# Kernel tuning notes

Measured on AMD Instinct MI355X. Metric: run time of the kernel, lower is better.

## Reference

```python
import jax, jax.numpy as jnp
import numpy as np
from jax.scipy.special import gammaln, logsumexp

N, P, K, R = 100000, 256, 64, 16

def setup_inputs() -> dict:
    key = jax.random.key(0)
    kx, km, kp = jax.random.split(key, 3)
    X = jax.random.normal(kx, (N, P), dtype=jnp.float32)
    X = X / jnp.linalg.norm(X, axis=1, keepdims=True)  # points on the sphere S^{p-1}
    M = jax.random.normal(km, (K, P, R), dtype=jnp.float32)
    pi = jax.random.normal(kp, (K,), dtype=jnp.float32)
    return {"X": X, "M": M, "pi": pi}

def reference(X, M, pi):
    p = X.shape[1]
    r = M.shape[-1]
    half_p = 0.5 * float(p)
    # log surface area constant of the ACG normalizer
    logSA = gammaln(half_p) - jnp.log(2.0) - half_p * jnp.log(jnp.pi)
    # D = I_r + M^T M per component: [K, r, r]
    D = jnp.eye(r, dtype=M.dtype) + jnp.einsum('kpr,kps->krs', M, M)
    _, log_det_D = jnp.linalg.slogdet(D)            # [K]
    Dinv = jnp.linalg.inv(D)                        # [K, r, r]
    XM = jnp.einsum('np,kpr->knr', X, M)            # [K, N, r]
    quad = jnp.einsum('knr,krs,kns->kn', XM, Dinv, XM)  # [K, N]
    pdf = 1.0 - quad                                # Woodbury: x^T Sigma^{-1} x for unit x
    log_acg_pdf = logSA - 0.5 * log_det_D[:, None] - half_p * jnp.log(pdf)
    density = log_acg_pdf + jax.nn.log_softmax(pi)[:, None]   # [K, N]
    loglik = jnp.sum(logsumexp(density, axis=0))
    return loglik
```

## Files before the change

kernel.cpp:

```cpp
#include <hip/hip_runtime.h>
#include <hip/hip_bf16.h>
#include <math.h>

#define NPTS 100000
#define NSTRIPE 1568
#define KCOMP 64

typedef float v4f __attribute__((ext_vector_type(4)));
typedef __bf16 v8bf __attribute__((ext_vector_type(8)));
typedef __bf16 v4bf __attribute__((ext_vector_type(4)));


__global__ __launch_bounds__(256) void prep_comp(const float* __restrict__ M,
                                                 const float* __restrict__ pi,
                                                 __bf16* __restrict__ Bt,
                                                 float* __restrict__ cvec,
                                                 float logSA) {
    __shared__ float Ml[256][16];
    __shared__ float S[16][17];
    __shared__ float sh_logpi;
    const int k = blockIdx.x, t = threadIdx.x;

    const float4* src = (const float4*)(M + (size_t)k * 4096 + (size_t)t * 16);
    float4 a0 = src[0], a1 = src[1], a2 = src[2], a3 = src[3];
    ((float4*)Ml[t])[0] = a0; ((float4*)Ml[t])[1] = a1;
    ((float4*)Ml[t])[2] = a2; ((float4*)Ml[t])[3] = a3;

    if (t < 64) {
        float v = pi[t];
        float mx = v;
        for (int off = 32; off; off >>= 1) mx = fmaxf(mx, __shfl_xor(mx, off));
        float e = __expf(v - mx);
        float s = e;
        for (int off = 32; off; off >>= 1) s += __shfl_xor(s, off);
        if (t == 0) sh_logpi = pi[k] - mx - logf(s);
    }
    __syncthreads();

    {
        int r = t >> 4, c = t & 15;
        float s = (r == c) ? 1.0f : 0.0f;
        for (int p = 0; p < 256; ++p) s += Ml[p][r] * Ml[p][c];
        S[r][c] = s;
    }
    __syncthreads();

    for (int j = 0; j < 16; ++j) {
        if (t == 0) S[j][j] = sqrtf(S[j][j]);
        __syncthreads();
        if (t > j && t < 16) S[t][j] = S[t][j] / S[j][j];
        __syncthreads();
        {
            int r = t >> 4, c = t & 15;
            if (r > j && c > j && c <= r) S[r][c] -= S[r][j] * S[c][j];
        }
        __syncthreads();
    }

    if (t == 0) {
        float ldet = 0.0f;
        for (int j = 0; j < 16; ++j) ldet += logf(S[j][j]);
        cvec[k] = logSA - ldet + sh_logpi;
    }

    float m[16] = {a0.x, a0.y, a0.z, a0.w, a1.x, a1.y, a1.z, a1.w,
                   a2.x, a2.y, a2.z, a2.w, a3.x, a3.y, a3.z, a3.w};
    float y[16];
#pragma unroll
    for (int r = 0; r < 16; ++r) {
        float v = m[r];
#pragma unroll
        for (int q = 0; q < r; ++q) v -= S[r][q] * y[q];
        y[r] = v / S[r][r];
    }
    const int cw = k >> 2, n = k & 3;
    const int ks = t >> 5, e = t & 7;
    const int lbase = ((t >> 3) & 3) * 16;
#pragma unroll
    for (int r = 0; r < 16; ++r) {
        const size_t off = (size_t)cw * 16384 + (size_t)ks * 2048 + (size_t)n * 512
                         + (size_t)(lbase + r) * 8 + e;
        Bt[off] = (__bf16)y[r];
    }
}

__global__ __launch_bounds__(256) void convert_X(const float* __restrict__ X,
                                                 __bf16* __restrict__ Xb) {
    __shared__ __bf16 T[64][264];
    const int st = blockIdx.x;
    const int n0 = st * 64;
    const int t = threadIdx.x;

#pragma unroll
    for (int j = 0; j < 16; ++j) {
        const int u = j * 256 + t;
        const int r = u >> 6, c4 = u & 63;
        const int n = n0 + r;
        float4 v = make_float4(0.f, 0.f, 0.f, 0.f);
        if (n < NPTS) v = ((const float4*)X)[(size_t)n * 64 + c4];
        v4bf o = {(__bf16)v.x, (__bf16)v.y, (__bf16)v.z, (__bf16)v.w};
        *(v4bf*)&T[r][c4 * 4] = o;
    }
    __syncthreads();

#pragma unroll
    for (int ks = 0; ks < 8; ++ks) {
        const int mh = t >> 6;
        const int l = t & 63;
        const int row = mh * 16 + (l & 15);
        const int col = ks * 32 + (l >> 4) * 8;
        v8bf val = *(const v8bf*)&T[row][col];
        const size_t off = (size_t)st * 16384 + (size_t)ks * 2048
                         + (size_t)mh * 512 + (size_t)l * 8;
        *(v8bf*)(Xb + off) = val;
    }
}

__global__ __launch_bounds__(256, 2) void gemm_density(const __bf16* __restrict__ Xb,
                                                       const __bf16* __restrict__ Bt,
                                                       const float* __restrict__ cvec,
                                                       float* __restrict__ out) {
    const int bid = blockIdx.x;
    const int xcd = bid & 7;
    const int w = threadIdx.x >> 6, lane = threadIdx.x & 63;
    const int widx = (bid >> 3) * 4 + w;
    if (widx >= 196) return;
    const int st = xcd * 196 + widx;
    const int laneoff = lane * 8;

    const __bf16* Ab = Xb + ((size_t)st << 14) + laneoff;
    v8bf af[8][4];
#pragma unroll
    for (int ks = 0; ks < 8; ++ks)
#pragma unroll
        for (int m = 0; m < 4; ++m) {
            af[ks][m] = *(const v8bf*)(Ab + ks * 2048 + m * 512);
            asm volatile("" : "+v"(af[ks][m]));
        }

    const __bf16* Bbase = Bt + laneoff;
#define LOADB(dst, cw_, ks_) do {                                                \
    const __bf16* _p = Bbase + ((size_t)(cw_) << 14) + (ks_) * 2048;             \
    _Pragma("unroll")                                                            \
    for (int n = 0; n < 4; ++n) dst[n] = *(const v8bf*)(_p + n * 512);           \
} while (0)
#define MFMA16(bg, ks) do {                                                      \
    _Pragma("unroll")                                                            \
    for (int m = 0; m < 4; ++m)                                                  \
        _Pragma("unroll")                                                        \
        for (int n = 0; n < 4; ++n)                                              \
            acc[m][n] = __builtin_amdgcn_mfma_f32_16x16x32_bf16(bg[n], af[ks][m], acc[m][n], 0, 0, 0); \
} while (0)

    const float4* cv4 = (const float4*)cvec;
    const v4f z4 = (v4f)(0.0f);

    v8bf bgA[4], bgB[4];
    LOADB(bgA, 0, 0);

    float mrun[4] = {-INFINITY, -INFINITY, -INFINITY, -INFINITY};
    float srun[4] = {0.f, 0.f, 0.f, 0.f};

#pragma unroll 1
    for (int cw = 0; cw < 16; ++cw) {
        v4f acc[4][4];
        LOADB(bgB, cw, 1);
#pragma unroll
        for (int m = 0; m < 4; ++m)
#pragma unroll
            for (int n = 0; n < 4; ++n)
                acc[m][n] = __builtin_amdgcn_mfma_f32_16x16x32_bf16(bgB[n] * (__bf16)0.f + bgA[n], af[0][m], z4, 0, 0, 0);
        LOADB(bgA, cw, 2);
        MFMA16(bgB, 1);
#pragma unroll
        for (int kp = 1; kp < 4; ++kp) {
            const int k0 = kp * 2, k1 = kp * 2 + 1;
            LOADB(bgB, cw, k1);
            MFMA16(bgA, k0);
            if (k1 < 7) { LOADB(bgA, cw, k1 + 1); }
            else if (cw < 15) { LOADB(bgA, cw + 1, 0); }
            MFMA16(bgB, k1);
        }

        const float4 cv = cv4[cw];
#pragma unroll
        for (int m = 0; m < 4; ++m) {
            float d[4];
#pragma unroll
            for (int n = 0; n < 4; ++n) {
                v4f qv = acc[m][n];
                float s = qv[0] * qv[0] + qv[1] * qv[1] + qv[2] * qv[2] + qv[3] * qv[3];
                s += __shfl_xor(s, 16);
                s += __shfl_xor(s, 32);
                const float c = (n == 0) ? cv.x : (n == 1) ? cv.y : (n == 2) ? cv.z : cv.w;
                d[n] = c - 128.0f * __logf(1.0f - s);
            }
            const float mt = fmaxf(fmaxf(d[0], d[1]), fmaxf(d[2], d[3]));
            const float mn = fmaxf(mrun[m], mt);
            srun[m] = srun[m] * __expf(mrun[m] - mn)
                    + __expf(d[0] - mn) + __expf(d[1] - mn)
                    + __expf(d[2] - mn) + __expf(d[3] - mn);
            mrun[m] = mn;
        }
    }
#undef LOADB
#undef MFMA16

    float tot = 0.f;
#pragma unroll
    for (int m = 0; m < 4; ++m) {
        const int pt = st * 64 + m * 16 + (lane & 15);
        const float lse = mrun[m] + __logf(srun[m]);
        tot += (pt < NPTS) ? lse : 0.f;
    }
    tot += __shfl_xor(tot, 1);
    tot += __shfl_xor(tot, 2);
    tot += __shfl_xor(tot, 4);
    tot += __shfl_xor(tot, 8);
    if (lane == 0) atomicAdd(out, tot);
}

extern "C" void kernel_launch(void* const* d_in, const int* in_sizes, int n_in,
                              void* d_out, int out_size, void* d_ws, size_t ws_size,
                              hipStream_t stream) {
    const float* X  = (const float*)d_in[0];
    const float* M  = (const float*)d_in[1];
    const float* pi = (const float*)d_in[2];
    float* out = (float*)d_out;

    char* ws = (char*)d_ws;
    __bf16* Xb   = (__bf16*)ws;
    __bf16* Bt   = (__bf16*)(ws + 51380224);
    float*  cvec = (float*)(ws + 51904512);

    const double half_p = 128.0;
    const float logSA = (float)(lgamma(half_p) - log(2.0) - half_p * log(M_PI));

    hipMemsetAsync(d_out, 0, sizeof(float), stream);
    prep_comp<<<64, 256, 0, stream>>>(M, pi, Bt, cvec, logSA);
    convert_X<<<1568, 256, 0, stream>>>(X, Xb);
    gemm_density<<<512, 256, 0, stream>>>(Xb, Bt, cvec, out);
}
```

Measured before the change: 148.1 us.

## Fuse fp32-to-bf16 conversion of X into GEMM kernel and drop convert pass

Removes the separate convert_X kernel and its bf16 staging buffer; each wave now loads its 64 rows of X directly as fp32 and converts them to bf16 MFMA fragments in registers. The B-fragment prefetch becomes a 4-deep ring buffer loaded two k-steps ahead, and the launch drops the XCD-aware block mapping, moving from 512 blocks to 392 blocks with occupancy hint 1. This avoids writing and re-reading a ~51MB intermediate and one kernel launch, at the cost of uncoalesced strided fp32 row loads and possibly lower occupancy.

```diff
diff --git a/kernel.cpp b/kernel.cpp
--- a/kernel.cpp
+++ b/kernel.cpp
@@ -3,12 +3,10 @@
 #include <math.h>
 
 #define NPTS 100000
-#define NSTRIPE 1568
 #define KCOMP 64
 
 typedef float v4f __attribute__((ext_vector_type(4)));
 typedef __bf16 v8bf __attribute__((ext_vector_type(8)));
-typedef __bf16 v4bf __attribute__((ext_vector_type(4)));
 
 
 __global__ __launch_bounds__(256) void prep_comp(const float* __restrict__ M,
@@ -84,102 +82,62 @@
     }
 }
 
-__global__ __launch_bounds__(256) void convert_X(const float* __restrict__ X,
-                                                 __bf16* __restrict__ Xb) {
-    __shared__ __bf16 T[64][264];
-    const int st = blockIdx.x;
-    const int n0 = st * 64;
-    const int t = threadIdx.x;
-
-#pragma unroll
-    for (int j = 0; j < 16; ++j) {
-        const int u = j * 256 + t;
-        const int r = u >> 6, c4 = u & 63;
-        const int n = n0 + r;
-        float4 v = make_float4(0.f, 0.f, 0.f, 0.f);
-        if (n < NPTS) v = ((const float4*)X)[(size_t)n * 64 + c4];
-        v4bf o = {(__bf16)v.x, (__bf16)v.y, (__bf16)v.z, (__bf16)v.w};
-        *(v4bf*)&T[r][c4 * 4] = o;
-    }
-    __syncthreads();
-
-#pragma unroll
-    for (int ks = 0; ks < 8; ++ks) {
-        const int mh = t >> 6;
-        const int l = t & 63;
-        const int row = mh * 16 + (l & 15);
-        const int col = ks * 32 + (l >> 4) * 8;
-        v8bf val = *(const v8bf*)&T[row][col];
-        const size_t off = (size_t)st * 16384 + (size_t)ks * 2048
-                         + (size_t)mh * 512 + (size_t)l * 8;
-        *(v8bf*)(Xb + off) = val;
-    }
-}
-
-__global__ __launch_bounds__(256, 2) void gemm_density(const __bf16* __restrict__ Xb,
+__global__ __launch_bounds__(256, 1) void gemm_density(const float* __restrict__ X,
                                                        const __bf16* __restrict__ Bt,
                                                        const float* __restrict__ cvec,
                                                        float* __restrict__ out) {
-    const int bid = blockIdx.x;
-    const int xcd = bid & 7;
-    const int w = threadIdx.x >> 6, lane = threadIdx.x & 63;
-    const int widx = (bid >> 3) * 4 + w;
-    if (widx >= 196) return;
-    const int st = xcd * 196 + widx;
-    const int laneoff = lane * 8;
+    const int st = blockIdx.x * 4 + (threadIdx.x >> 6);
+    const int lane = threadIdx.x & 63;
+    const int lo = lane & 15, hi = lane >> 4;
+    const int n0 = st * 64;
 
-    const __bf16* Ab = Xb + ((size_t)st << 14) + laneoff;
     v8bf af[8][4];
 #pragma unroll
-    for (int ks = 0; ks < 8; ++ks)
+    for (int m = 0; m < 4; ++m) {
+        const int row = min(n0 + m * 16 + lo, NPTS - 1);
+        const float* rp = X + (size_t)row * 256 + hi * 8;
 #pragma unroll
-        for (int m = 0; m < 4; ++m) {
-            af[ks][m] = *(const v8bf*)(Ab + ks * 2048 + m * 512);
-            asm volatile("" : "+v"(af[ks][m]));
+        for (int ks = 0; ks < 8; ++ks) {
+            const float4 f0 = *(const float4*)(rp + ks * 32);
+            const float4 f1 = *(const float4*)(rp + ks * 32 + 4);
+            v8bf v;
+            v[0] = (__bf16)f0.x; v[1] = (__bf16)f0.y; v[2] = (__bf16)f0.z; v[3] = (__bf16)f0.w;
+            v[4] = (__bf16)f1.x; v[5] = (__bf16)f1.y; v[6] = (__bf16)f1.z; v[7] = (__bf16)f1.w;
+            af[ks][m] = v;
         }
+    }
 
-    const __bf16* Bbase = Bt + laneoff;
-#define LOADB(dst, cw_, ks_) do {                                                \
-    const __bf16* _p = Bbase + ((size_t)(cw_) << 14) + (ks_) * 2048;             \
-    _Pragma("unroll")                                                            \
-    for (int n = 0; n < 4; ++n) dst[n] = *(const v8bf*)(_p + n * 512);           \
-} while (0)
-#define MFMA16(bg, ks) do {                                                      \
-    _Pragma("unroll")                                                            \
-    for (int m = 0; m < 4; ++m)                                                  \
-        _Pragma("unroll")                                                        \
-        for (int n = 0; n < 4; ++n)                                              \
-            acc[m][n] = __builtin_amdgcn_mfma_f32_16x16x32_bf16(bg[n], af[ks][m], acc[m][n], 0, 0, 0); \
+    const __bf16* Bb = Bt + lane * 8;
+#define LOADB(dst, cw_, ks_) do {                                        \
+    const __bf16* _p = Bb + ((size_t)(cw_) << 14) + ((size_t)(ks_) << 11); \
+    dst[0] = *(const v8bf*)(_p);                                         \
+    dst[1] = *(const v8bf*)(_p + 512);                                   \
+    dst[2] = *(const v8bf*)(_p + 1024);                                  \
+    dst[3] = *(const v8bf*)(_p + 1536);                                  \
 } while (0)
 
-    const float4* cv4 = (const float4*)cvec;
-    const v4f z4 = (v4f)(0.0f);
-
-    v8bf bgA[4], bgB[4];
-    LOADB(bgA, 0, 0);
+    v8bf bg[4][4];
+    LOADB(bg[0], 0, 0);
+    LOADB(bg[1], 0, 1);
 
     float mrun[4] = {-INFINITY, -INFINITY, -INFINITY, -INFINITY};
     float srun[4] = {0.f, 0.f, 0.f, 0.f};
+    const float4* cv4 = (const float4*)cvec;
 
 #pragma unroll 1
     for (int cw = 0; cw < 16; ++cw) {
-        v4f acc[4][4];
-        LOADB(bgB, cw, 1);
+        v4f acc[4][4] = {};
 #pragma unroll
-        for (int m = 0; m < 4; ++m)
+        for (int ks = 0; ks < 8; ++ks) {
+            const int pk = ks + 2;
+            const int pcw = (pk < 8) ? cw : ((cw + 1) & 15);
+            LOADB(bg[pk & 3], pcw, pk & 7);
 #pragma unroll
-            for (int n = 0; n < 4; ++n)
-                acc[m][n] = __builtin_amdgcn_mfma_f32_16x16x32_bf16(bgB[n] * (__bf16)0.f + bgA[n], af[0][m], z4, 0, 0, 0);
-        LOADB(bgA, cw, 2);
-        MFMA16(bgB, 1);
+            for (int m = 0; m < 4; ++m)
 #pragma unroll
-        for (int kp = 1; kp < 4; ++kp) {
-            const int k0 = kp * 2, k1 = kp * 2 + 1;
-            LOADB(bgB, cw, k1);
-            MFMA16(bgA, k0);
-            if (k1 < 7) { LOADB(bgA, cw, k1 + 1); }
-            else if (cw < 15) { LOADB(bgA, cw + 1, 0); }
-            MFMA16(bgB, k1);
+                for (int n = 0; n < 4; ++n)
+                    acc[m][n] = __builtin_amdgcn_mfma_f32_16x16x32_bf16(
+                        bg[ks & 3][n], af[ks][m], acc[m][n], 0, 0, 0);
         }
 
         const float4 cv = cv4[cw];
@@ -204,12 +162,11 @@
         }
     }
 #undef LOADB
-#undef MFMA16
 
     float tot = 0.f;
 #pragma unroll
     for (int m = 0; m < 4; ++m) {
-        const int pt = st * 64 + m * 16 + (lane & 15);
+        const int pt = n0 + m * 16 + lo;
         const float lse = mrun[m] + __logf(srun[m]);
         tot += (pt < NPTS) ? lse : 0.f;
     }
@@ -229,15 +186,13 @@
     float* out = (float*)d_out;
 
     char* ws = (char*)d_ws;
-    __bf16* Xb   = (__bf16*)ws;
-    __bf16* Bt   = (__bf16*)(ws + 51380224);
-    float*  cvec = (float*)(ws + 51904512);
+    __bf16* Bt   = (__bf16*)ws;
+    float*  cvec = (float*)(ws + 524288);
 
     const double half_p = 128.0;
     const float logSA = (float)(lgamma(half_p) - log(2.0) - half_p * log(M_PI));
 
     hipMemsetAsync(d_out, 0, sizeof(float), stream);
     prep_comp<<<64, 256, 0, stream>>>(M, pi, Bt, cvec, logSA);
-    convert_X<<<1568, 256, 0, stream>>>(X, Xb);
-    gemm_density<<<512, 256, 0, stream>>>(Xb, Bt, cvec, out);
+    gemm_density<<<392, 256, 0, stream>>>(X, Bt, cvec, out);
 }
```

Measured after the change: 178.6 us. 20.6% more time.
